# Optimization experiments

Hardware: AMD Instinct MI355X
Metric: run time of the kernel (lower is better)

## Reference

```python
import jax, jax.numpy as jnp
import numpy as np

B, NH, T, N, D = 4, 8, 2048, 512, 128
THETA = 2.0 ** 16
GAMMA = 0.995


def setup_inputs() -> dict:
    key = jax.random.key(0)
    kq, kv, ks = jax.random.split(key, 3)
    Q = jax.random.normal(kq, (B, NH, T, N), jnp.float32)
    V = jax.random.normal(kv, (B, NH, T, D), jnp.float32)
    S_prev = 0.01 * jax.random.normal(ks, (B, NH, N, D), jnp.float32)
    # get_freqs(N, theta=2**16): per-channel inverse frequencies
    freqs = jnp.asarray(1.0 / THETA ** (np.arange(N, dtype=np.float32) / N), jnp.float32)
    gamma = jnp.float32(GAMMA)
    return {"Q": Q, "V": V, "S_prev": S_prev, "freqs": freqs, "gamma": gamma}


def _rope(phases, v):
    """Rotary embedding with per-channel phases. phases broadcasts against v's
    last two dims (T, N); rotate-half formulation."""
    cos, sin = jnp.cos(phases), jnp.sin(phases)
    half = v.shape[-1] // 2
    v_rot = jnp.concatenate([-v[..., half:], v[..., :half]], axis=-1)
    return v * cos + v_rot * sin


def reference(Q, V, S_prev, freqs, gamma):
    # Q: (B,nh,T,N)  V: (B,nh,T,D)  S_prev: (B,nh,N,D)
    t_len = Q.shape[2]
    phases = jnp.arange(t_len, dtype=freqs.dtype)[:, None] * freqs[None, :]  # (T,N)
    QR = _rope(phases[None, None], Q)  # K == Q per the module's assert

    q_seq = jnp.moveaxis(QR, 2, 0)  # (T,B,nh,N)
    v_seq = jnp.moveaxis(V, 2, 0)   # (T,B,nh,D)

    def step(S, qv):
        q_t, v_t = qv
        out_t = jnp.einsum('bhn,bhnd->bhd', q_t, S)          # read before write
        S_new = (S + jnp.einsum('bhn,bhd->bhnd', q_t, v_t)) * gamma  # write + decay
        return S_new, out_t

    S_final, outs = jax.lax.scan(step, S_prev, (q_seq, v_seq))
    output = jnp.moveaxis(outs, 0, 2)  # (B,nh,T,D)
    return output, S_final
```

## Files before the change

kernel.cpp:

```cpp
#include <hip/hip_runtime.h>
#include <hip/hip_bf16.h>

typedef __attribute__((ext_vector_type(8))) short short8;
typedef __attribute__((ext_vector_type(4))) float f32x4;

#define MFMA16(a,b,c) __builtin_amdgcn_mfma_f32_16x16x32_bf16((a),(b),(c),0,0,0)

constexpr int BHn = 32;
constexpr int Tn  = 2048;
constexpr int Nn  = 512;
constexpr int Dn  = 128;
constexpr int CHn = 128;
constexpr int NCH = Tn / CHn;

static __device__ __forceinline__ unsigned short f2b(float x){
  __hip_bfloat16 h = __float2bfloat16(x);
  return *reinterpret_cast<unsigned short*>(&h);
}

__global__ __launch_bounds__(256) void rope_k(const float* __restrict__ Q,
                                              const float* __restrict__ freqs,
                                              unsigned short* __restrict__ QR){
  int gid = blockIdx.x * 256 + threadIdx.x;
  int np  = gid & 255;
  int t   = gid >> 8;
  float tf = (float)t;
  float f1 = freqs[np], f2 = freqs[np + 256];
  float s1, c1, s2, c2;
  sincosf(tf * f1, &s1, &c1);
  sincosf(tf * f2, &s2, &c2);
  size_t off = (size_t)t * Nn + np;
  for (int bh = 0; bh < BHn; ++bh){
    size_t base = (size_t)bh * Tn * Nn + off;
    float q1 = Q[base], q2 = Q[base + 256];
    QR[base]       = f2b(q1 * c1 - q2 * s1);
    QR[base + 256] = f2b(q2 * c2 + q1 * s2);
  }
}

__device__ __forceinline__ short8 ldfrag(const unsigned short* buf, int rowbase, int k0, int ld, int lane){
  int row = rowbase + (lane & 15);
  int col = (k0 + ((lane >> 4) << 3)) ^ ((row & 7) << 3);
  return *reinterpret_cast<const short8*>(buf + row * ld + col);
}
__device__ __forceinline__ short8 gfrag(const unsigned short* Qc, int rowbase, int k0, int lane){
  return *reinterpret_cast<const short8*>(
      Qc + (size_t)(rowbase + (lane & 15)) * Nn + k0 + ((lane >> 4) << 3));
}
__device__ __forceinline__ void stage_Rs(unsigned short* Rs, uint4 a, uint4 b, int dt, int n0){
  *reinterpret_cast<uint4*>(&Rs[ dt      * 512 + (n0 ^ (( dt      & 7) << 3))]) = a;
  *reinterpret_cast<uint4*>(&Rs[(dt + 1) * 512 + (n0 ^ (((dt + 1) & 7) << 3))]) = b;
}

__global__ __launch_bounds__(256) void pt_k(const unsigned short* __restrict__ QR,
                                            const float* __restrict__ gammap,
                                            unsigned short* __restrict__ Pt){
  __shared__ __align__(16) unsigned short Rs[64 * 512];
  __shared__ float gpow[129];
  const int tid = threadIdx.x, w = tid >> 6, lane = tid & 63;
  const int bh = blockIdx.x & 31, cc = (blockIdx.x >> 5) & 15, sub = blockIdx.x >> 9;
  const int ro = sub * 64;
  if (tid < 129) gpow[tid] = powf(gammap[0], (float)tid);
  const unsigned short* Qc = QR + (size_t)bh * Tn * Nn + (size_t)(cc * CHn + ro) * Nn;
  #pragma unroll
  for (int i = 0; i < 8; ++i){
    int p  = tid + i * 256;
    int dt = (p >> 6) << 1, n0 = (p & 63) << 3;
    const unsigned short* src = Qc + (size_t)dt * Nn + n0;
    uint4 a = *reinterpret_cast<const uint4*>(src);
    uint4 b = *reinterpret_cast<const uint4*>(src + Nn);
    stage_Rs(Rs, a, b, dt, n0);
  }
  __syncthreads();
  f32x4 p0 = {0.f,0.f,0.f,0.f}, p1 = p0, p2 = p0;
  for (int kb = 0; kb < 16; ++kb){
    int k0 = kb * 32;
    if (w == 0){
      short8 f0 = ldfrag(Rs,  0, k0, 512, lane);
      short8 f1 = ldfrag(Rs, 16, k0, 512, lane);
      p0 = MFMA16(f0, f0, p0);
      p1 = MFMA16(f1, f0, p1);
      p2 = MFMA16(f1, f1, p2);
    } else if (w == 1){
      short8 f0 = ldfrag(Rs,  0, k0, 512, lane);
      short8 f1 = ldfrag(Rs, 16, k0, 512, lane);
      short8 f2 = ldfrag(Rs, 32, k0, 512, lane);
      p0 = MFMA16(f2, f0, p0);
      p1 = MFMA16(f2, f1, p1);
      p2 = MFMA16(f2, f2, p2);
    } else if (w == 2){
      short8 f0 = ldfrag(Rs,  0, k0, 512, lane);
      short8 f1 = ldfrag(Rs, 16, k0, 512, lane);
      short8 f3 = ldfrag(Rs, 48, k0, 512, lane);
      p0 = MFMA16(f3, f0, p0);
      p1 = MFMA16(f3, f1, p1);
    } else {
      short8 f2 = ldfrag(Rs, 32, k0, 512, lane);
      short8 f3 = ldfrag(Rs, 48, k0, 512, lane);
      p0 = MFMA16(f3, f2, p0);
      p1 = MFMA16(f3, f3, p1);
    }
  }
  unsigned short* Pq = Pt + (size_t)(bh * NCH + cc) * (CHn * CHn);
  auto pwrite = [&](f32x4 pa, int tI, int tJ){
    int j  = tJ * 16 + (lane & 15);
    int i0 = tI * 16 + ((lane >> 4) << 2);
    #pragma unroll
    for (int r = 0; r < 4; ++r){
      int i = i0 + r;
      float v = (j < i) ? pa[r] * gpow[i + ro] : 0.f;
      Pq[(i + ro) * CHn + ro + (j ^ ((i & 7) << 3))] = f2b(v);
    }
  };
  if      (w == 0){ pwrite(p0,0,0); pwrite(p1,1,0); pwrite(p2,1,1); pwrite(p0,0,1); }
  else if (w == 1){ pwrite(p0,2,0); pwrite(p1,2,1); pwrite(p2,2,2); pwrite(p0,0,2); }
  else if (w == 2){ pwrite(p0,3,0); pwrite(p1,3,1); pwrite(p0,0,3); pwrite(p1,1,2); }
  else            { pwrite(p0,3,2); pwrite(p1,3,3); pwrite(p0,1,3); pwrite(p1,2,3); }
}

__global__ __launch_bounds__(256) void po_k(const unsigned short* __restrict__ QR,
                                            const float* __restrict__ gammap,
                                            unsigned short* __restrict__ Pt){
  __shared__ float gpow[129];
  const int tid = threadIdx.x, w = tid >> 6, lane = tid & 63;
  const int bh = blockIdx.x & 31, cc = blockIdx.x >> 5;
  if (tid < 129) gpow[tid] = powf(gammap[0], (float)tid);
  __syncthreads();
  const unsigned short* QB = QR + (size_t)bh * Tn * Nn + (size_t)(cc * CHn) * Nn;
  const unsigned short* QA = QB + (size_t)64 * Nn;
  f32x4 acc[4] = {{0.f,0.f,0.f,0.f},{0.f,0.f,0.f,0.f},{0.f,0.f,0.f,0.f},{0.f,0.f,0.f,0.f}};
  for (int kb = 0; kb < 16; ++kb){
    int k0 = kb * 32;
    short8 fa = gfrag(QA, w * 16, k0, lane);
    #pragma unroll
    for (int t = 0; t < 4; ++t){
      short8 fb = gfrag(QB, t * 16, k0, lane);
      acc[t] = MFMA16(fa, fb, acc[t]);
    }
  }
  unsigned short* Pq = Pt + (size_t)(bh * NCH + cc) * (CHn * CHn);
  #pragma unroll
  for (int t = 0; t < 4; ++t){
    int j  = t * 16 + (lane & 15);
    int i0 = w * 16 + ((lane >> 4) << 2);
    #pragma unroll
    for (int r = 0; r < 4; ++r){
      int i = i0 + r;
      float v = acc[t][r] * gpow[64 + i];
      Pq[(64 + i) * CHn + (j ^ ((i & 7) << 3))] = f2b(v);
    }
  }
}

__global__ __launch_bounds__(512, 1) void lattn_main(
    const unsigned short* __restrict__ QR,
    const unsigned short* __restrict__ Pt,
    const float* __restrict__ V,
    const float* __restrict__ S_prev,
    const float* __restrict__ gammap,
    float* __restrict__ Out,
    float* __restrict__ Sfin)
{
  __shared__ __align__(16) unsigned short SbTs[16 * 512];
  __shared__ __align__(16) unsigned short VTs[2][16 * 128];
  __shared__ float gpow[129], gpinv[129];

  const int tid  = threadIdx.x;
  const int w    = tid >> 6;
  const int lane = tid & 63;
  const int bh   = blockIdx.x & 31;
  const int dch  = blockIdx.x >> 5;
  const int d0   = dch * 16;
  const float g  = gammap[0];

  const unsigned short* QRbh = QR + (size_t)bh * Tn * Nn;
  const unsigned short* Ptbh = Pt + (size_t)bh * NCH * (CHn * CHn);
  const float* Vbh = V + (size_t)bh * Tn * Dn;

  if (tid < 129){
    gpow[tid]  = powf(g,  (float)tid);
    gpinv[tid] = powf(g, -(float)tid);
  }

  const int snt = (w < 4) ? 2 : 6;
  const int sb  = (w < 4) ? w * 2 : 8 + (w - 4) * 6;
  f32x4 st[6];
  #pragma unroll
  for (int j = 0; j < 6; ++j) if (j < snt){
    int n = (sb + j) * 16 + (lane & 15);
    st[j] = *reinterpret_cast<const f32x4*>(
        S_prev + (size_t)bh * Nn * Dn + (size_t)n * Dn + d0 + ((lane >> 4) << 2));
  }
  __syncthreads();
  const float g128 = gpow[128];

  #pragma unroll
  for (int j = 0; j < 6; ++j) if (j < snt){
    int n  = (sb + j) * 16 + (lane & 15);
    int dl = (lane >> 4) << 2;
    #pragma unroll
    for (int r = 0; r < 4; ++r){
      int d = dl + r;
      SbTs[d * 512 + (n ^ ((d & 7) << 3))] = f2b(st[j][r]);
    }
  }
  {
    int dtv = tid >> 2, dp0 = (tid & 3) << 2;
    f32x4 v4 = *reinterpret_cast<const f32x4*>(Vbh + (size_t)dtv * Dn + d0 + dp0);
    float sc = gpinv[dtv];
    #pragma unroll
    for (int r = 0; r < 4; ++r){
      int d = dp0 + r;
      VTs[0][d * 128 + (dtv ^ ((d & 7) << 3))] = f2b(v4[r] * sc);
    }
  }
  __syncthreads();

  for (int c = 0; c < NCH; ++c){
    const int t0 = c * CHn;
    const int vb = c & 1;
    const bool pf = (c + 1 < NCH);
    const unsigned short* Qc = QRbh + (size_t)t0 * Nn;

    f32x4 va4 = {0.f, 0.f, 0.f, 0.f};
    const int dtv_ = tid >> 2, dp0_ = (tid & 3) << 2;
    if (pf)
      va4 = *reinterpret_cast<const f32x4*>(Vbh + (size_t)(t0 + CHn + dtv_) * Dn + d0 + dp0_);

    if (w < 4){
      const int it0 = w, it1 = w + 4;
      f32x4 o0 = {0.f,0.f,0.f,0.f}, o1 = o0;
      for (int kb = 0; kb < 16; ++kb){
        int k0 = kb * 32;
        short8 fs = ldfrag(SbTs, 0, k0, 512, lane);
        short8 fa = gfrag(Qc, it0 * 16, k0, lane);
        short8 fb = gfrag(Qc, it1 * 16, k0, lane);
        o0 = MFMA16(fs, fa, o0);
        o1 = MFMA16(fs, fb, o1);
      }
      float g0 = gpow[it0 * 16 + (lane & 15)];
      float g1 = gpow[it1 * 16 + (lane & 15)];
      #pragma unroll
      for (int r = 0; r < 4; ++r){ o0[r] *= g0; o1[r] *= g1; }
      const unsigned short* Pq = Ptbh + (size_t)c * (CHn * CHn);
      #pragma unroll
      for (int ks = 0; ks < 4; ++ks){
        short8 av = ldfrag(VTs[vb], 0, ks * 32, 128, lane);
        if (ks < 2){
          short8 b0 = ldfrag(Pq, it0 * 16, ks * 32, CHn, lane);
          o0 = MFMA16(av, b0, o0);
        }
        short8 b1 = ldfrag(Pq, it1 * 16, ks * 32, CHn, lane);
        o1 = MFMA16(av, b1, o1);
      }
      int ti0 = t0 + it0 * 16 + (lane & 15);
      int ti1 = t0 + it1 * 16 + (lane & 15);
      *reinterpret_cast<f32x4*>(
          Out + (size_t)bh * Tn * Dn + (size_t)ti0 * Dn + d0 + ((lane >> 4) << 2)) = o0;
      *reinterpret_cast<f32x4*>(
          Out + (size_t)bh * Tn * Dn + (size_t)ti1 * Dn + d0 + ((lane >> 4) << 2)) = o1;
    }
    #pragma unroll
    for (int ks = 0; ks < 4; ++ks){
      short8 av = ldfrag(VTs[vb], 0, ks * 32, 128, lane);
      #pragma unroll
      for (int j = 0; j < 6; ++j) if (j < snt){
        int n = (sb + j) * 16 + (lane & 15);
        const unsigned short* col = Qc + (size_t)(ks * 32 + ((lane >> 4) << 3)) * Nn + n;
        short8 bn;
        #pragma unroll
        for (int e = 0; e < 8; ++e) bn[e] = (short)col[(size_t)e * Nn];
        st[j] = MFMA16(av, bn, st[j]);
      }
    }
    #pragma unroll
    for (int j = 0; j < 6; ++j) if (j < snt)
      #pragma unroll
      for (int r = 0; r < 4; ++r) st[j][r] *= g128;
    __syncthreads();

    #pragma unroll
    for (int j = 0; j < 6; ++j) if (j < snt){
      int n  = (sb + j) * 16 + (lane & 15);
      int dl = (lane >> 4) << 2;
      #pragma unroll
      for (int r = 0; r < 4; ++r){
        int d = dl + r;
        SbTs[d * 512 + (n ^ ((d & 7) << 3))] = f2b(st[j][r]);
      }
    }
    if (pf){
      float sc = gpinv[dtv_];
      #pragma unroll
      for (int r = 0; r < 4; ++r){
        int d = dp0_ + r;
        VTs[vb ^ 1][d * 128 + (dtv_ ^ ((d & 7) << 3))] = f2b(va4[r] * sc);
      }
    }
    __syncthreads();
  }

  #pragma unroll
  for (int j = 0; j < 6; ++j) if (j < snt){
    int n = (sb + j) * 16 + (lane & 15);
    *reinterpret_cast<f32x4*>(
        Sfin + (size_t)bh * Nn * Dn + (size_t)n * Dn + d0 + ((lane >> 4) << 2)) = st[j];
  }
}

extern "C" void kernel_launch(void* const* d_in, const int* in_sizes, int n_in,
                              void* d_out, int out_size, void* d_ws, size_t ws_size,
                              hipStream_t stream){
  const float* Q      = (const float*)d_in[0];
  const float* V      = (const float*)d_in[1];
  const float* S_prev = (const float*)d_in[2];
  const float* freqs  = (const float*)d_in[3];
  const float* gamma  = (const float*)d_in[4];
  float* Out  = (float*)d_out;
  float* Sfin = Out + (size_t)BHn * Tn * Dn;
  unsigned short* QR = (unsigned short*)d_ws;
  unsigned short* Pt = QR + (size_t)BHn * Tn * Nn;

  rope_k<<<2048, 256, 0, stream>>>(Q, freqs, QR);
  pt_k<<<1024, 256, 0, stream>>>(QR, gamma, Pt);
  po_k<<<512, 256, 0, stream>>>(QR, gamma, Pt);
  lattn_main<<<256, 512, 0, stream>>>(QR, Pt, V, S_prev, gamma, Out, Sfin);
}
```

Measured before the change: 219.6 us.

## Precompute per-chunk state updates in a parallel kernel to shorten the serial scan

Adds a u_k kernel that computes each chunk's state increment U = QR^T·(gamma-scaled V) for all chunks in parallel and writes it to workspace as bf16. A new lattn_s main kernel then only adds U and decays the register state per chunk, so the per-chunk state-update MFMAs leave the serial loop. This costs an extra kernel launch plus about 64MB of bf16 U written and read back. It also adds bf16 rounding of U before accumulation. The new path runs only when the workspace is large enough, otherwise the old kernel is used.

```diff
diff --git a/kernel.cpp b/kernel.cpp
--- a/kernel.cpp
+++ b/kernel.cpp
@@ -3,6 +3,7 @@
 
 typedef __attribute__((ext_vector_type(8))) short short8;
 typedef __attribute__((ext_vector_type(4))) float f32x4;
+typedef __attribute__((ext_vector_type(4))) unsigned short ushort4v;
 
 #define MFMA16(a,b,c) __builtin_amdgcn_mfma_f32_16x16x32_bf16((a),(b),(c),0,0,0)
 
@@ -16,6 +17,12 @@
 static __device__ __forceinline__ unsigned short f2b(float x){
   __hip_bfloat16 h = __float2bfloat16(x);
   return *reinterpret_cast<unsigned short*>(&h);
+}
+static __device__ __forceinline__ float b2f(unsigned short u){
+  unsigned v = (unsigned)u << 16;
+  float f;
+  __builtin_memcpy(&f, &v, 4);
+  return f;
 }
 
 __global__ __launch_bounds__(256) void rope_k(const float* __restrict__ Q,
@@ -152,6 +159,197 @@
   }
 }
 
+__global__ __launch_bounds__(512) void u_k(const unsigned short* __restrict__ QR,
+                                           const float* __restrict__ V,
+                                           const float* __restrict__ gammap,
+                                           unsigned short* __restrict__ U){
+  __shared__ __align__(16) unsigned short VTs[16 * 128];
+  __shared__ float gpinv[129];
+  const int tid = threadIdx.x, w = tid >> 6, lane = tid & 63;
+  const int bh = blockIdx.x & 31, cc = (blockIdx.x >> 5) & 15, dch = blockIdx.x >> 9;
+  const int d0 = dch * 16;
+  if (tid < 129) gpinv[tid] = powf(gammap[0], -(float)tid);
+  __syncthreads();
+  {
+    int dtv = tid >> 2, dp0 = (tid & 3) << 2;
+    f32x4 v4 = *reinterpret_cast<const f32x4*>(
+        V + ((size_t)bh * Tn + cc * CHn + dtv) * Dn + d0 + dp0);
+    float sc = gpinv[dtv];
+    #pragma unroll
+    for (int r = 0; r < 4; ++r){
+      int d = dp0 + r;
+      VTs[d * 128 + (dtv ^ ((d & 7) << 3))] = f2b(v4[r] * sc);
+    }
+  }
+  __syncthreads();
+  const unsigned short* Qc = QR + (size_t)bh * Tn * Nn + (size_t)(cc * CHn) * Nn;
+  const int sb = w * 4;
+  f32x4 st[4] = {{0.f,0.f,0.f,0.f},{0.f,0.f,0.f,0.f},{0.f,0.f,0.f,0.f},{0.f,0.f,0.f,0.f}};
+  #pragma unroll
+  for (int ks = 0; ks < 4; ++ks){
+    short8 av = ldfrag(VTs, 0, ks * 32, 128, lane);
+    #pragma unroll
+    for (int j = 0; j < 4; ++j){
+      int n = (sb + j) * 16 + (lane & 15);
+      const unsigned short* col = Qc + (size_t)(ks * 32 + ((lane >> 4) << 3)) * Nn + n;
+      short8 bn;
+      #pragma unroll
+      for (int e = 0; e < 8; ++e) bn[e] = (short)col[(size_t)e * Nn];
+      st[j] = MFMA16(av, bn, st[j]);
+    }
+  }
+  unsigned short* Uc = U + (size_t)(bh * NCH + cc) * Nn * Dn;
+  #pragma unroll
+  for (int j = 0; j < 4; ++j){
+    int n = (sb + j) * 16 + (lane & 15);
+    ushort4v o;
+    #pragma unroll
+    for (int r = 0; r < 4; ++r) o[r] = f2b(st[j][r]);
+    *reinterpret_cast<ushort4v*>(Uc + (size_t)n * Dn + d0 + ((lane >> 4) << 2)) = o;
+  }
+}
+
+__global__ __launch_bounds__(512, 1) void lattn_s(
+    const unsigned short* __restrict__ QR,
+    const unsigned short* __restrict__ Pt,
+    const unsigned short* __restrict__ U,
+    const float* __restrict__ V,
+    const float* __restrict__ S_prev,
+    const float* __restrict__ gammap,
+    float* __restrict__ Out,
+    float* __restrict__ Sfin)
+{
+  __shared__ __align__(16) unsigned short SbTs[16 * 512];
+  __shared__ __align__(16) unsigned short VTs[2][16 * 128];
+  __shared__ float gpow[129], gpinv[129];
+
+  const int tid  = threadIdx.x;
+  const int w    = tid >> 6;
+  const int lane = tid & 63;
+  const int bh   = blockIdx.x & 31;
+  const int dch  = blockIdx.x >> 5;
+  const int d0   = dch * 16;
+  const float g  = gammap[0];
+
+  const unsigned short* QRbh = QR + (size_t)bh * Tn * Nn;
+  const unsigned short* Ptbh = Pt + (size_t)bh * NCH * (CHn * CHn);
+  const unsigned short* Ubh  = U  + (size_t)bh * NCH * Nn * Dn;
+  const float* Vbh = V + (size_t)bh * Tn * Dn;
+
+  if (tid < 129){
+    gpow[tid]  = powf(g,  (float)tid);
+    gpinv[tid] = powf(g, -(float)tid);
+  }
+
+  const int sb = w * 4;
+  f32x4 st[4];
+  #pragma unroll
+  for (int j = 0; j < 4; ++j){
+    int n = (sb + j) * 16 + (lane & 15);
+    st[j] = *reinterpret_cast<const f32x4*>(
+        S_prev + (size_t)bh * Nn * Dn + (size_t)n * Dn + d0 + ((lane >> 4) << 2));
+  }
+  __syncthreads();
+  const float g128 = gpow[128];
+
+  #pragma unroll
+  for (int j = 0; j < 4; ++j){
+    int n  = (sb + j) * 16 + (lane & 15);
+    int dl = (lane >> 4) << 2;
+    #pragma unroll
+    for (int r = 0; r < 4; ++r){
+      int d = dl + r;
+      SbTs[d * 512 + (n ^ ((d & 7) << 3))] = f2b(st[j][r]);
+    }
+  }
+  {
+    int dtv = tid >> 2, dp0 = (tid & 3) << 2;
+    f32x4 v4 = *reinterpret_cast<const f32x4*>(Vbh + (size_t)dtv * Dn + d0 + dp0);
+    float sc = gpinv[dtv];
+    #pragma unroll
+    for (int r = 0; r < 4; ++r){
+      int d = dp0 + r;
+      VTs[0][d * 128 + (dtv ^ ((d & 7) << 3))] = f2b(v4[r] * sc);
+    }
+  }
+  __syncthreads();
+
+  for (int c = 0; c < NCH; ++c){
+    const int t0 = c * CHn;
+    const int vb = c & 1;
+    const bool pf = (c + 1 < NCH);
+    const unsigned short* Qc = QRbh + (size_t)t0 * Nn;
+
+    f32x4 va4 = {0.f, 0.f, 0.f, 0.f};
+    const int dtv_ = tid >> 2, dp0_ = (tid & 3) << 2;
+    if (pf)
+      va4 = *reinterpret_cast<const f32x4*>(Vbh + (size_t)(t0 + CHn + dtv_) * Dn + d0 + dp0_);
+
+    {
+      f32x4 o = {0.f, 0.f, 0.f, 0.f};
+      for (int kb = 0; kb < 16; ++kb){
+        int k0 = kb * 32;
+        short8 fs = ldfrag(SbTs, 0, k0, 512, lane);
+        short8 fi = gfrag(Qc, w * 16, k0, lane);
+        o = MFMA16(fs, fi, o);
+      }
+      float gi = gpow[w * 16 + (lane & 15)];
+      #pragma unroll
+      for (int r = 0; r < 4; ++r) o[r] *= gi;
+      const unsigned short* Pq = Ptbh + (size_t)c * (CHn * CHn);
+      const int nks = (w >> 1) + 1;
+      #pragma unroll
+      for (int ks = 0; ks < 4; ++ks) if (ks < nks){
+        short8 av = ldfrag(VTs[vb], 0, ks * 32, 128, lane);
+        short8 bp = ldfrag(Pq, w * 16, ks * 32, CHn, lane);
+        o = MFMA16(av, bp, o);
+      }
+      int ti = t0 + w * 16 + (lane & 15);
+      *reinterpret_cast<f32x4*>(
+          Out + (size_t)bh * Tn * Dn + (size_t)ti * Dn + d0 + ((lane >> 4) << 2)) = o;
+    }
+    {
+      const unsigned short* Uc = Ubh + (size_t)c * Nn * Dn;
+      #pragma unroll
+      for (int j = 0; j < 4; ++j){
+        int n = (sb + j) * 16 + (lane & 15);
+        ushort4v u4 = *reinterpret_cast<const ushort4v*>(
+            Uc + (size_t)n * Dn + d0 + ((lane >> 4) << 2));
+        #pragma unroll
+        for (int r = 0; r < 4; ++r) st[j][r] = (st[j][r] + b2f(u4[r])) * g128;
+      }
+    }
+    __syncthreads();
+
+    #pragma unroll
+    for (int j = 0; j < 4; ++j){
+      int n  = (sb + j) * 16 + (lane & 15);
+      int dl = (lane >> 4) << 2;
+      #pragma unroll
+      for (int r = 0; r < 4; ++r){
+        int d = dl + r;
+        SbTs[d * 512 + (n ^ ((d & 7) << 3))] = f2b(st[j][r]);
+      }
+    }
+    if (pf){
+      float sc = gpinv[dtv_];
+      #pragma unroll
+      for (int r = 0; r < 4; ++r){
+        int d = dp0_ + r;
+        VTs[vb ^ 1][d * 128 + (dtv_ ^ ((d & 7) << 3))] = f2b(va4[r] * sc);
+      }
+    }
+    __syncthreads();
+  }
+
+  #pragma unroll
+  for (int j = 0; j < 4; ++j){
+    int n = (sb + j) * 16 + (lane & 15);
+    *reinterpret_cast<f32x4*>(
+        Sfin + (size_t)bh * Nn * Dn + (size_t)n * Dn + d0 + ((lane >> 4) << 2)) = st[j];
+  }
+}
+
 __global__ __launch_bounds__(512, 1) void lattn_main(
     const unsigned short* __restrict__ QR,
     const unsigned short* __restrict__ Pt,
@@ -318,11 +516,21 @@
   const float* gamma  = (const float*)d_in[4];
   float* Out  = (float*)d_out;
   float* Sfin = Out + (size_t)BHn * Tn * Dn;
+
+  const size_t QRs = (size_t)BHn * Tn * Nn;
+  const size_t Pts = (size_t)BHn * NCH * CHn * CHn;
+  const size_t Us  = (size_t)BHn * NCH * Nn * Dn;
   unsigned short* QR = (unsigned short*)d_ws;
-  unsigned short* Pt = QR + (size_t)BHn * Tn * Nn;
+  unsigned short* Pt = QR + QRs;
+  unsigned short* U  = Pt + Pts;
 
   rope_k<<<2048, 256, 0, stream>>>(Q, freqs, QR);
   pt_k<<<1024, 256, 0, stream>>>(QR, gamma, Pt);
   po_k<<<512, 256, 0, stream>>>(QR, gamma, Pt);
-  lattn_main<<<256, 512, 0, stream>>>(QR, Pt, V, S_prev, gamma, Out, Sfin);
-}
+  if (ws_size >= 2 * (QRs + Pts + Us)){
+    u_k<<<4096, 512, 0, stream>>>(QR, V, gamma, U);
+    lattn_s<<<256, 512, 0, stream>>>(QR, Pt, U, V, S_prev, gamma, Out, Sfin);
+  } else {
+    lattn_main<<<256, 512, 0, stream>>>(QR, Pt, V, S_prev, gamma, Out, Sfin);
+  }
+}
```

New measurement: 296.4 us. 1.35x slower.

## Merge intra-chunk P diagonal and off-diagonal kernels into one load-balanced kernel

Applied to the files above, without the earlier changes.

Replaces the two kernels that built the per-chunk decayed QQ^T lower-triangular matrix (pt_k with shared-memory staging for diagonal blocks, po_k for the off-diagonal block) with one kernel. Each of the four waves computes two complementary row tiles of the 8x8 lower-triangle tile grid so work is balanced, and explicitly zeroes the upper tiles. This removes a launch and the LDS staging, but fragments are now read straight from global memory (L2) with more redundant loads per block.

```diff
diff --git a/kernel.cpp b/kernel.cpp
--- a/kernel.cpp
+++ b/kernel.cpp
@@ -47,78 +47,8 @@
   return *reinterpret_cast<const short8*>(
       Qc + (size_t)(rowbase + (lane & 15)) * Nn + k0 + ((lane >> 4) << 3));
 }
-__device__ __forceinline__ void stage_Rs(unsigned short* Rs, uint4 a, uint4 b, int dt, int n0){
-  *reinterpret_cast<uint4*>(&Rs[ dt      * 512 + (n0 ^ (( dt      & 7) << 3))]) = a;
-  *reinterpret_cast<uint4*>(&Rs[(dt + 1) * 512 + (n0 ^ (((dt + 1) & 7) << 3))]) = b;
-}
-
-__global__ __launch_bounds__(256) void pt_k(const unsigned short* __restrict__ QR,
-                                            const float* __restrict__ gammap,
-                                            unsigned short* __restrict__ Pt){
-  __shared__ __align__(16) unsigned short Rs[64 * 512];
-  __shared__ float gpow[129];
-  const int tid = threadIdx.x, w = tid >> 6, lane = tid & 63;
-  const int bh = blockIdx.x & 31, cc = (blockIdx.x >> 5) & 15, sub = blockIdx.x >> 9;
-  const int ro = sub * 64;
-  if (tid < 129) gpow[tid] = powf(gammap[0], (float)tid);
-  const unsigned short* Qc = QR + (size_t)bh * Tn * Nn + (size_t)(cc * CHn + ro) * Nn;
-  #pragma unroll
-  for (int i = 0; i < 8; ++i){
-    int p  = tid + i * 256;
-    int dt = (p >> 6) << 1, n0 = (p & 63) << 3;
-    const unsigned short* src = Qc + (size_t)dt * Nn + n0;
-    uint4 a = *reinterpret_cast<const uint4*>(src);
-    uint4 b = *reinterpret_cast<const uint4*>(src + Nn);
-    stage_Rs(Rs, a, b, dt, n0);
-  }
-  __syncthreads();
-  f32x4 p0 = {0.f,0.f,0.f,0.f}, p1 = p0, p2 = p0;
-  for (int kb = 0; kb < 16; ++kb){
-    int k0 = kb * 32;
-    if (w == 0){
-      short8 f0 = ldfrag(Rs,  0, k0, 512, lane);
-      short8 f1 = ldfrag(Rs, 16, k0, 512, lane);
-      p0 = MFMA16(f0, f0, p0);
-      p1 = MFMA16(f1, f0, p1);
-      p2 = MFMA16(f1, f1, p2);
-    } else if (w == 1){
-      short8 f0 = ldfrag(Rs,  0, k0, 512, lane);
-      short8 f1 = ldfrag(Rs, 16, k0, 512, lane);
-      short8 f2 = ldfrag(Rs, 32, k0, 512, lane);
-      p0 = MFMA16(f2, f0, p0);
-      p1 = MFMA16(f2, f1, p1);
-      p2 = MFMA16(f2, f2, p2);
-    } else if (w == 2){
-      short8 f0 = ldfrag(Rs,  0, k0, 512, lane);
-      short8 f1 = ldfrag(Rs, 16, k0, 512, lane);
-      short8 f3 = ldfrag(Rs, 48, k0, 512, lane);
-      p0 = MFMA16(f3, f0, p0);
-      p1 = MFMA16(f3, f1, p1);
-    } else {
-      short8 f2 = ldfrag(Rs, 32, k0, 512, lane);
-      short8 f3 = ldfrag(Rs, 48, k0, 512, lane);
-      p0 = MFMA16(f3, f2, p0);
-      p1 = MFMA16(f3, f3, p1);
-    }
-  }
-  unsigned short* Pq = Pt + (size_t)(bh * NCH + cc) * (CHn * CHn);
-  auto pwrite = [&](f32x4 pa, int tI, int tJ){
-    int j  = tJ * 16 + (lane & 15);
-    int i0 = tI * 16 + ((lane >> 4) << 2);
-    #pragma unroll
-    for (int r = 0; r < 4; ++r){
-      int i = i0 + r;
-      float v = (j < i) ? pa[r] * gpow[i + ro] : 0.f;
-      Pq[(i + ro) * CHn + ro + (j ^ ((i & 7) << 3))] = f2b(v);
-    }
-  };
-  if      (w == 0){ pwrite(p0,0,0); pwrite(p1,1,0); pwrite(p2,1,1); pwrite(p0,0,1); }
-  else if (w == 1){ pwrite(p0,2,0); pwrite(p1,2,1); pwrite(p2,2,2); pwrite(p0,0,2); }
-  else if (w == 2){ pwrite(p0,3,0); pwrite(p1,3,1); pwrite(p0,0,3); pwrite(p1,1,2); }
-  else            { pwrite(p0,3,2); pwrite(p1,3,3); pwrite(p0,1,3); pwrite(p1,2,3); }
-}
-
-__global__ __launch_bounds__(256) void po_k(const unsigned short* __restrict__ QR,
+
+__global__ __launch_bounds__(256) void pd_k(const unsigned short* __restrict__ QR,
                                             const float* __restrict__ gammap,
                                             unsigned short* __restrict__ Pt){
   __shared__ float gpow[129];
@@ -126,28 +56,61 @@
   const int bh = blockIdx.x & 31, cc = blockIdx.x >> 5;
   if (tid < 129) gpow[tid] = powf(gammap[0], (float)tid);
   __syncthreads();
-  const unsigned short* QB = QR + (size_t)bh * Tn * Nn + (size_t)(cc * CHn) * Nn;
-  const unsigned short* QA = QB + (size_t)64 * Nn;
-  f32x4 acc[4] = {{0.f,0.f,0.f,0.f},{0.f,0.f,0.f,0.f},{0.f,0.f,0.f,0.f},{0.f,0.f,0.f,0.f}};
+  const unsigned short* Qc = QR + (size_t)bh * Tn * Nn + (size_t)(cc * CHn) * Nn;
+
+  int tiA, ntA, tiB, ntB;
+  if      (w == 0){ tiA = 0; ntA = 1; tiB = 7; ntB = 8; }
+  else if (w == 1){ tiA = 1; ntA = 2; tiB = 6; ntB = 7; }
+  else if (w == 2){ tiA = 2; ntA = 3; tiB = 5; ntB = 6; }
+  else            { tiA = 3; ntA = 4; tiB = 4; ntB = 5; }
+
+  f32x4 accA[4], accB[8];
+  #pragma unroll
+  for (int t = 0; t < 4; ++t) accA[t] = {0.f, 0.f, 0.f, 0.f};
+  #pragma unroll
+  for (int t = 0; t < 8; ++t) accB[t] = {0.f, 0.f, 0.f, 0.f};
+
   for (int kb = 0; kb < 16; ++kb){
     int k0 = kb * 32;
-    short8 fa = gfrag(QA, w * 16, k0, lane);
-    #pragma unroll
-    for (int t = 0; t < 4; ++t){
-      short8 fb = gfrag(QB, t * 16, k0, lane);
-      acc[t] = MFMA16(fa, fb, acc[t]);
-    }
-  }
+    short8 faA = gfrag(Qc, tiA * 16, k0, lane);
+    short8 faB = gfrag(Qc, tiB * 16, k0, lane);
+    #pragma unroll
+    for (int tj = 0; tj < 8; ++tj){
+      short8 fb = gfrag(Qc, tj * 16, k0, lane);
+      if (tj < ntA) accA[tj] = MFMA16(faA, fb, accA[tj]);
+      if (tj < ntB) accB[tj] = MFMA16(faB, fb, accB[tj]);
+    }
+  }
+
   unsigned short* Pq = Pt + (size_t)(bh * NCH + cc) * (CHn * CHn);
-  #pragma unroll
-  for (int t = 0; t < 4; ++t){
-    int j  = t * 16 + (lane & 15);
-    int i0 = w * 16 + ((lane >> 4) << 2);
-    #pragma unroll
-    for (int r = 0; r < 4; ++r){
-      int i = i0 + r;
-      float v = acc[t][r] * gpow[64 + i];
-      Pq[(64 + i) * CHn + (j ^ ((i & 7) << 3))] = f2b(v);
+  auto pw = [&](f32x4 pa, int ti, int tj, bool diag){
+    int jg = tj * 16 + (lane & 15);
+    int i0 = ti * 16 + ((lane >> 4) << 2);
+    #pragma unroll
+    for (int r = 0; r < 4; ++r){
+      int ig = i0 + r;
+      float v = (!diag || (jg < ig)) ? pa[r] * gpow[ig] : 0.f;
+      Pq[ig * CHn + (jg ^ ((ig & 7) << 3))] = f2b(v);
+    }
+  };
+  #pragma unroll
+  for (int tj = 0; tj < 4; ++tj) if (tj < ntA) pw(accA[tj], tiA, tj, tj == ntA - 1);
+  #pragma unroll
+  for (int tj = 0; tj < 8; ++tj) if (tj < ntB) pw(accB[tj], tiB, tj, tj == ntB - 1);
+
+  int zi[3], zj[3];
+  if      (w == 0){ zi[0]=4; zj[0]=5; zi[1]=4; zj[1]=6; zi[2]=4; zj[2]=7; }
+  else if (w == 1){ zi[0]=5; zj[0]=6; zi[1]=5; zj[1]=7; zi[2]=0; zj[2]=1; }
+  else if (w == 2){ zi[0]=6; zj[0]=7; zi[1]=0; zj[1]=2; zi[2]=0; zj[2]=3; }
+  else            { zi[0]=1; zj[0]=2; zi[1]=1; zj[1]=3; zi[2]=2; zj[2]=3; }
+  #pragma unroll
+  for (int z = 0; z < 3; ++z){
+    int jg = zj[z] * 16 + (lane & 15);
+    int i0 = zi[z] * 16 + ((lane >> 4) << 2);
+    #pragma unroll
+    for (int r = 0; r < 4; ++r){
+      int ig = i0 + r;
+      Pq[ig * CHn + (jg ^ ((ig & 7) << 3))] = 0;
     }
   }
 }
@@ -318,11 +281,11 @@
   const float* gamma  = (const float*)d_in[4];
   float* Out  = (float*)d_out;
   float* Sfin = Out + (size_t)BHn * Tn * Dn;
+
   unsigned short* QR = (unsigned short*)d_ws;
   unsigned short* Pt = QR + (size_t)BHn * Tn * Nn;
 
   rope_k<<<2048, 256, 0, stream>>>(Q, freqs, QR);
-  pt_k<<<1024, 256, 0, stream>>>(QR, gamma, Pt);
-  po_k<<<512, 256, 0, stream>>>(QR, gamma, Pt);
+  pd_k<<<512, 256, 0, stream>>>(QR, gamma, Pt);
   lattn_main<<<256, 512, 0, stream>>>(QR, Pt, V, S_prev, gamma, Out, Sfin);
 }
```

Result: no change. 216.9 us (-1.2%).
